# Kernel tuning notes

Measured on AMD Instinct MI355X. Metric: run time of the kernel, lower is better.

Reference implementation:

```python
import jax, jax.numpy as jnp
import numpy as np

EPS = 1e-8
XLAMBDA = 9.0  # hard-coded in i2t_scores call to Encoding_sim


def setup_inputs() -> dict:
    key = jax.random.key(0)
    ks = jax.random.split(key, 12)
    I, C, N, S, W, D = 48, 48, 1, 36, 32, 1024  # n_image, n_caption, views, regions, words, embed
    NB, HID, P, OUT, KK = 64, 256, 2, 1, 8      # num_block, hid_dim, Pieces, out_dim, n_kernels
    return {
        "images": jax.random.normal(ks[0], (I, N, S, D), jnp.float32),
        "captions": jax.random.normal(ks[1], (C, N, W, D), jnp.float32),
        "cap_lens": jax.random.randint(ks[2], (C,), 1, W + 1),
        "delt": jax.random.uniform(ks[3], (NB,), jnp.float32, 0.5, 1.0),
        "W1": jax.random.normal(ks[4], (NB, NB), jnp.float32) * 0.1,
        "b1": jnp.zeros((NB,), jnp.float32),
        "W2": jax.random.normal(ks[5], (NB, NB), jnp.float32) * 0.1,
        "b2": jnp.zeros((NB,), jnp.float32),
        "conv_W": jax.random.normal(ks[6], (KK, NB, NB), jnp.float32) * 0.1,
        "conv_b": jnp.zeros((NB,), jnp.float32),
        "Wm": jax.random.normal(ks[7], (NB, HID * P), jnp.float32) * 0.1,
        "bm": jnp.zeros((HID * P,), jnp.float32),
        "V": jax.random.normal(ks[8], (OUT, HID), jnp.float32) * 0.1,
        "g": jnp.ones((OUT,), jnp.float32),
        "bo": jnp.zeros((OUT,), jnp.float32),
    }


def _one_view(img, cap, delt, W1, b1, W2, b2, conv_W, conv_b, Wm, bm, V, g, bo):
    # img: (I, S, D) regions; cap: (C, W, D) words. All captions processed at full
    # length (the torch double loop over captions/views is fully vectorized).
    I, S, D = img.shape
    C = cap.shape[0]
    NB = delt.shape[0]
    db = D // NB
    # inter_relations with K=caption words, Q=image regions
    a = jax.nn.leaky_relu(jnp.einsum('cwd,isd->ciws', cap, img), 0.1)  # (C,I,W,S)
    a = a / (jnp.sqrt(jnp.sum(a * a, axis=-1, keepdims=True)) + EPS)   # l2norm over regions (dim=2)
    attn = jax.nn.softmax(XLAMBDA * jnp.swapaxes(a, -1, -2), axis=-1)  # (C,I,S,W) softmax over words
    # weighted caption context per region
    ctx = jnp.einsum('cisw,cwd->cisd', attn, cap)                      # (C,I,S,D)
    # blockwise cosine similarity vector, scaled by learned delt
    q = img.reshape(I, S, NB, db)[None]                                # (1,I,S,NB,db)
    cb = ctx.reshape(C, I, S, NB, db)
    w12 = jnp.sum(q * cb, axis=-1)
    nrm = jnp.linalg.norm(q, axis=-1) * jnp.linalg.norm(cb, axis=-1)
    sim = (w12 / jnp.maximum(nrm, EPS)) * delt                         # (C,I,S,NB)
    # WeightNetwork: learned region-region adjacency
    f1 = sim @ W1.T + b1
    f2 = sim @ W2.T + b2
    gw = jax.nn.softmax(jnp.einsum('cisn,citn->cist', f1, f2), axis=-1)  # (C,I,S,S)
    # VisualConvolution message passing: aggregate neighbors, mix with kernel bank
    msg = jnp.einsum('cist,citn->cisn', gw, sim)                       # (C,I,S,NB)
    conv = jnp.einsum('cisn,knm->cism', msg, conv_W) / conv_W.shape[0] + conv_b
    # MeanOut: linear to hid*Pieces, mean over pieces
    HID = V.shape[1]
    P = Wm.shape[1] // HID
    h = (conv @ Wm + bm).reshape(C, I, S, HID, P).mean(axis=-1)        # (C,I,S,HID)
    # weight-normalized output linear + tanh, then mean over regions
    Wn = g[:, None] * V / jnp.linalg.norm(V, axis=1, keepdims=True)
    y = jnp.tanh(h @ Wn.T + bo)                                        # (C,I,S,OUT)
    return jnp.mean(y.reshape(C, I, -1), axis=-1).T                    # (I,C)


def reference(images, captions, cap_lens, delt, W1, b1, W2, b2, conv_W, conv_b,
              Wm, bm, V, g, bo):
    # cap_lens: the ragged per-caption loop is uniformized to max length (see notes)
    f = lambda img, cap: _one_view(img, cap, delt, W1, b1, W2, b2, conv_W, conv_b,
                                   Wm, bm, V, g, bo)
    return jax.vmap(f, in_axes=(1, 1))(images, captions)  # (N, n_image, n_caption)
```

## Files before the change

### kernel.cpp

```cpp
#include <hip/hip_runtime.h>

#define EPSF 1e-8f

constexpr int NI = 48, NC = 48, S = 36, W = 32, D = 1024, NB = 64;
constexpr int CH = 64;
constexpr int NCH = D / CH;

typedef _Float16 half8 __attribute__((ext_vector_type(8)));
typedef _Float16 half4 __attribute__((ext_vector_type(4)));
typedef float f32x4 __attribute__((ext_vector_type(4)));

__device__ __forceinline__ f32x4 mfma16(half8 a, half8 b, f32x4 c) {
  return __builtin_amdgcn_mfma_f32_16x16x32_f16(a, b, c, 0, 0, 0);
}

constexpr size_t OFF_CAPTH = 17408;
constexpr size_t SZ_CAPT   = (size_t)48 * 32 * 1024 * 2;
constexpr size_t OFF_CAPTL = OFF_CAPTH + SZ_CAPT;
constexpr size_t OFF_L     = OFF_CAPTL + SZ_CAPT;
constexpr size_t SZ_L      = (size_t)1536 * 1728 * 4;
constexpr size_t OFF_DQ    = OFF_L + SZ_L;
constexpr size_t SZ_DQ     = (size_t)48 * 64 * 36 * 4;
constexpr size_t WS_NEED   = OFF_DQ + SZ_DQ;

__global__ __launch_bounds__(256) void prep_kernel(
    const float* __restrict__ W1, const float* __restrict__ b1,
    const float* __restrict__ W2,
    const float* __restrict__ convW, const float* __restrict__ convB,
    const float* __restrict__ Wm, const float* __restrict__ bm,
    const float* __restrict__ V, const float* __restrict__ g,
    const float* __restrict__ bo, float* __restrict__ ws) {
  __shared__ float sW1[64][68];
  __shared__ float sW2[64][68];
  __shared__ float wn[256];
  __shared__ float wv[64];
  __shared__ float vscale;
  const int t = threadIdx.x;
  for (int q = t; q < 2048; q += 256) {
    const int m = q >> 10, r = (q >> 4) & 63, c4 = (q & 15) * 4;
    const float* src = (m == 0 ? W1 : W2) + r * 64 + c4;
    float4 v = *reinterpret_cast<const float4*>(src);
    float* dst = (m == 0) ? &sW1[r][c4] : &sW2[r][c4];
    dst[0] = v.x; dst[1] = v.y; dst[2] = v.z; dst[3] = v.w;
  }
  if (t == 0) {
    float s = 0.f;
    for (int h = 0; h < 256; ++h) s += V[h] * V[h];
    vscale = g[0] / sqrtf(s);
  }
  __syncthreads();
  wn[t] = V[t] * vscale;
  __syncthreads();
  if (t < 64) {
    float acc = 0.f;
    for (int h = 0; h < 256; ++h)
      acc += 0.5f * (Wm[t * 512 + 2 * h] + Wm[t * 512 + 2 * h + 1]) * wn[h];
    wv[t] = acc;
  }
  __syncthreads();
  if (t < 64) {
    float acc = 0.f;
    for (int m = 0; m < 64; ++m) {
      float ce = 0.f;
      for (int k = 0; k < 8; ++k) ce += convW[k * 4096 + t * 64 + m];
      acc += 0.125f * ce * wv[m];
    }
    ws[t] = acc;
  }
  if (t == 0) {
    float bh = 0.f;
    for (int h = 0; h < 256; ++h) bh += 0.5f * (bm[2 * h] + bm[2 * h + 1]) * wn[h];
    float bc = 0.f;
    for (int m = 0; m < 64; ++m) bc += convB[m] * wv[m];
    ws[64] = bh + bc + bo[0];
  }
  if (t < 64) {
    float a = 0.f;
    for (int k = 0; k < 64; ++k) a += b1[k] * sW2[k][t];
    ws[66 + t] = a;
  }
  {
    const int i = t >> 2, j0 = (t & 3) * 16;
    float acc[16];
#pragma unroll
    for (int jj = 0; jj < 16; ++jj) acc[jj] = 0.f;
    for (int k = 0; k < 64; ++k) {
      const float w1v = sW1[k][i];
#pragma unroll
      for (int jj = 0; jj < 16; ++jj) acc[jj] += w1v * sW2[k][j0 + jj];
    }
    _Float16* wsM = reinterpret_cast<_Float16*>(ws + 132);
#pragma unroll
    for (int jj = 0; jj < 16; ++jj) {
      const float x = acc[jj];
      const _Float16 h = (_Float16)x;
      wsM[i * 64 + j0 + jj] = h;
      wsM[4096 + i * 64 + j0 + jj] = (_Float16)(x - (float)h);
    }
  }
}

__global__ __launch_bounds__(256) void setup_kernel(
    const float* __restrict__ captions, const float* __restrict__ images,
    const float* __restrict__ W1, const float* __restrict__ b1,
    const float* __restrict__ W2,
    const float* __restrict__ convW, const float* __restrict__ convB,
    const float* __restrict__ Wm, const float* __restrict__ bm,
    const float* __restrict__ V, const float* __restrict__ g,
    const float* __restrict__ bo,
    float* __restrict__ ws, _Float16* __restrict__ capTH,
    _Float16* __restrict__ capTL, float* __restrict__ dqT) {
  __shared__ union {
    struct { float sW1[64][68]; float sW2[64][68]; float wn[256]; float wv[64]; float vscale; } p;
    struct { _Float16 tH[64][40]; _Float16 tL[64][40]; } cc;
  } SM;
  const int t = threadIdx.x;
  const int bx = blockIdx.x;
  if (bx < 768) {
    const int c = bx >> 4, chn = bx & 15, d0 = chn * 64;
    for (int q = t; q < 512; q += 256) {
      const int w = q >> 4, c4 = (q & 15) * 4;
      const size_t gi = ((size_t)c * 32 + w) * 1024 + d0 + c4;
      float4 v = *reinterpret_cast<const float4*>(captions + gi);
      half4 hh, ll;
      hh[0] = (_Float16)v.x; ll[0] = (_Float16)(v.x - (float)hh[0]);
      hh[1] = (_Float16)v.y; ll[1] = (_Float16)(v.y - (float)hh[1]);
      hh[2] = (_Float16)v.z; ll[2] = (_Float16)(v.z - (float)hh[2]);
      hh[3] = (_Float16)v.w; ll[3] = (_Float16)(v.w - (float)hh[3]);
#pragma unroll
      for (int j = 0; j < 4; ++j) { SM.cc.tH[c4 + j][w] = hh[j]; SM.cc.tL[c4 + j][w] = ll[j]; }
    }
    __syncthreads();
    for (int q = t; q < 512; q += 256) {
      const int hl = q >> 8, dd = (q >> 2) & 63, w8 = (q & 3) * 8;
      half8 v = *reinterpret_cast<const half8*>(hl ? &SM.cc.tL[dd][w8] : &SM.cc.tH[dd][w8]);
      _Float16* dst = (hl ? capTL : capTH) + ((size_t)c * 1024 + d0 + dd) * 32 + w8;
      *reinterpret_cast<half8*>(dst) = v;
    }
  } else if (bx < 816) {
    const int i = bx - 768;
    for (int u = t; u < 2304; u += 256) {
      const int s = u >> 6, nb = u & 63;
      const float* p = images + ((size_t)i * 36 + s) * 1024 + nb * 16;
      float a = 0.f;
#pragma unroll
      for (int j = 0; j < 16; j += 4) {
        f32x4 v = *reinterpret_cast<const f32x4*>(p + j);
        a += v[0] * v[0] + v[1] * v[1] + v[2] * v[2] + v[3] * v[3];
      }
      dqT[((size_t)i * 64 + nb) * 36 + s] = a;
    }
  } else {
    for (int q = t; q < 2048; q += 256) {
      const int m = q >> 10, r = (q >> 4) & 63, c4 = (q & 15) * 4;
      const float* src = (m == 0 ? W1 : W2) + r * 64 + c4;
      float4 v = *reinterpret_cast<const float4*>(src);
      float* dst = (m == 0) ? &SM.p.sW1[r][c4] : &SM.p.sW2[r][c4];
      dst[0] = v.x; dst[1] = v.y; dst[2] = v.z; dst[3] = v.w;
    }
    if (t == 0) {
      float s = 0.f;
      for (int h = 0; h < 256; ++h) s += V[h] * V[h];
      SM.p.vscale = g[0] / sqrtf(s);
    }
    __syncthreads();
    SM.p.wn[t] = V[t] * SM.p.vscale;
    __syncthreads();
    if (t < 64) {
      float acc = 0.f;
      for (int h = 0; h < 256; ++h)
        acc += 0.5f * (Wm[t * 512 + 2 * h] + Wm[t * 512 + 2 * h + 1]) * SM.p.wn[h];
      SM.p.wv[t] = acc;
    }
    __syncthreads();
    if (t < 64) {
      float acc = 0.f;
      for (int m = 0; m < 64; ++m) {
        float ce = 0.f;
        for (int k = 0; k < 8; ++k) ce += convW[k * 4096 + t * 64 + m];
        acc += 0.125f * ce * SM.p.wv[m];
      }
      ws[t] = acc;
    }
    if (t == 0) {
      float bh = 0.f;
      for (int h = 0; h < 256; ++h) bh += 0.5f * (bm[2 * h] + bm[2 * h + 1]) * SM.p.wn[h];
      float bc = 0.f;
      for (int m = 0; m < 64; ++m) bc += convB[m] * SM.p.wv[m];
      ws[64] = bh + bc + bo[0];
    }
    if (t < 64) {
      float a = 0.f;
      for (int k = 0; k < 64; ++k) a += b1[k] * SM.p.sW2[k][t];
      ws[66 + t] = a;
    }
    {
      const int i = t >> 2, j0 = (t & 3) * 16;
      float acc[16];
#pragma unroll
      for (int jj = 0; jj < 16; ++jj) acc[jj] = 0.f;
      for (int k = 0; k < 64; ++k) {
        const float w1v = SM.p.sW1[k][i];
#pragma unroll
        for (int jj = 0; jj < 16; ++jj) acc[jj] += w1v * SM.p.sW2[k][j0 + jj];
      }
      _Float16* wsM = reinterpret_cast<_Float16*>(ws + 132);
#pragma unroll
      for (int jj = 0; jj < 16; ++jj) {
        const float x = acc[jj];
        const _Float16 h = (_Float16)x;
        wsM[i * 64 + j0 + jj] = h;
        wsM[4096 + i * 64 + j0 + jj] = (_Float16)(x - (float)h);
      }
    }
  }
}

__global__ __launch_bounds__(256, 3) void gemmL(
    const float* __restrict__ captions, const float* __restrict__ images,
    float* __restrict__ L) {
  __shared__ _Float16 sA[2][64][72];
  __shared__ _Float16 sB[2][96][72];
  const int t = threadIdx.x;
  const int lane = t & 63, wid = t >> 6;
  const int c = lane & 15, g = lane >> 4;
  const int bm = blockIdx.x / 18, bn = blockIdx.x % 18;
  const int m0 = bm * 64, n0 = bn * 96;
  const int wm = wid & 1, wn = wid >> 1;

  f32x4 acc[2][3] = {};
  f32x4 pfA[4], pfB[6];
  auto LD = [&](int ch) {
#pragma unroll
    for (int k = 0; k < 4; ++k) {
      const int u = t + k * 256;
      const int row = u >> 4, c4 = (u & 15) * 4;
      pfA[k] = *reinterpret_cast<const f32x4*>(captions + (size_t)(m0 + row) * 1024 + ch * 64 + c4);
    }
#pragma unroll
    for (int k = 0; k < 6; ++k) {
      const int u = t + k * 256;
      const int row = u >> 4, c4 = (u & 15) * 4;
      pfB[k] = *reinterpret_cast<const f32x4*>(images + (size_t)(n0 + row) * 1024 + ch * 64 + c4);
    }
  };
  auto ST = [&]() {
#pragma unroll
    for (int k = 0; k < 4; ++k) {
      const int u = t + k * 256;
      const int row = u >> 4, c4 = (u & 15) * 4;
      half4 hh, ll;
#pragma unroll
      for (int j = 0; j < 4; ++j) {
        const float x = pfA[k][j];
        hh[j] = (_Float16)x;
        ll[j] = (_Float16)(x - (float)hh[j]);
      }
      *reinterpret_cast<half4*>(&sA[0][row][c4]) = hh;
      *reinterpret_cast<half4*>(&sA[1][row][c4]) = ll;
    }
#pragma unroll
    for (int k = 0; k < 6; ++k) {
      const int u = t + k * 256;
      const int row = u >> 4, c4 = (u & 15) * 4;
      half4 hh, ll;
#pragma unroll
      for (int j = 0; j < 4; ++j) {
        const float x = pfB[k][j];
        hh[j] = (_Float16)x;
        ll[j] = (_Float16)(x - (float)hh[j]);
      }
      *reinterpret_cast<half4*>(&sB[0][row][c4]) = hh;
      *reinterpret_cast<half4*>(&sB[1][row][c4]) = ll;
    }
  };
  LD(0);
  for (int ch = 0; ch < NCH; ++ch) {
    __syncthreads();
    ST();
    if (ch < NCH - 1) LD(ch + 1);
    __syncthreads();
#pragma unroll
    for (int ks = 0; ks < 2; ++ks) {
      const int ko = ks * 32 + g * 8;
      half8 ah[2], al[2], bh[3], bl[3];
#pragma unroll
      for (int mt = 0; mt < 2; ++mt) {
        ah[mt] = *reinterpret_cast<const half8*>(&sA[0][wm * 32 + mt * 16 + c][ko]);
        al[mt] = *reinterpret_cast<const half8*>(&sA[1][wm * 32 + mt * 16 + c][ko]);
      }
#pragma unroll
      for (int nt = 0; nt < 3; ++nt) {
        bh[nt] = *reinterpret_cast<const half8*>(&sB[0][wn * 48 + nt * 16 + c][ko]);
        bl[nt] = *reinterpret_cast<const half8*>(&sB[1][wn * 48 + nt * 16 + c][ko]);
      }
#pragma unroll
      for (int mt = 0; mt < 2; ++mt)
#pragma unroll
        for (int nt = 0; nt < 3; ++nt) {
          acc[mt][nt] = mfma16(ah[mt], bh[nt], acc[mt][nt]);
          acc[mt][nt] = mfma16(ah[mt], bl[nt], acc[mt][nt]);
          acc[mt][nt] = mfma16(al[mt], bh[nt], acc[mt][nt]);
        }
    }
  }
#pragma unroll
  for (int mt = 0; mt < 2; ++mt)
#pragma unroll
    for (int nt = 0; nt < 3; ++nt)
#pragma unroll
      for (int r = 0; r < 4; ++r) {
        const int m = m0 + wm * 32 + mt * 16 + 4 * g + r;
        const int n = n0 + wn * 48 + nt * 16 + c;
        float x = acc[mt][nt][r];
        x = x > 0.f ? x : 0.1f * x;
        L[(size_t)m * 1728 + n] = x;
      }
}

__device__ __forceinline__ int swz(int row, int nbyte) {
  return row * 128 + (nbyte ^ ((row & 7) << 4));
}

__global__ __launch_bounds__(256, 5) void i2t_sim4(
    const float* __restrict__ images,
    const _Float16* __restrict__ capTH, const _Float16* __restrict__ capTL,
    const float* __restrict__ L, const float* __restrict__ dqT,
    const float* __restrict__ delt, const float* __restrict__ ws,
    float* __restrict__ out) {
  __shared__ union {
    float La[32][41];
    _Float16 yhl[2][2304];
  } UA;
  __shared__ union {
    _Float16 attn[2][36][40];
    float G[36][49];
  } UB;
  __shared__ _Float16 simS[2][2304];
  __shared__ float wrcp[32];
  __shared__ float sDelt[64], sCv[64], sU[64];
  __shared__ float sP[36], sScv[36], sRed[36];
  __shared__ float sBconst;

  const int t = threadIdx.x;
  const int lane = t & 63, wid = t >> 6;
  const int c = lane & 15, g = lane >> 4;
  const int bid = blockIdx.x;
  const int xcd = bid & 7, l = bid >> 3;
  const int ci = (xcd >> 1) * 12 + (l % 12);
  const int ii = (xcd & 1) * 24 + (l / 12);

  if (t < 64) { sDelt[t] = delt[t]; sCv[t] = ws[t]; sU[t] = ws[66 + t]; }
  if (t == 64) sBconst = ws[64];

#pragma unroll
  for (int k = 0; k < 2; ++k) {
    const int u = t + k * 256;
    if (u < 288) {
      const int w = u / 9, q4 = (u % 9) * 4;
      f32x4 x = *reinterpret_cast<const f32x4*>(
          L + (size_t)(ci * 32 + w) * 1728 + (size_t)ii * 36 + q4);
      *reinterpret_cast<f32x4*>(&UA.La[w][q4]) = x;
    }
  }
  __syncthreads();
  if (t < 32) {
    float s = 0.f;
    for (int ss = 0; ss < 36; ++ss) { const float v = UA.La[t][ss]; s += v * v; }
    wrcp[t] = 1.f / (sqrtf(s) + EPSF);
  }
  __syncthreads();
  if (t < 36) {
    float lw[32];
    float m = -1e30f;
#pragma unroll
    for (int w = 0; w < 32; ++w) {
      const float v = 9.f * UA.La[w][t] * wrcp[w];
      lw[w] = v;
      m = fmaxf(m, v);
    }
    float sum = 0.f;
#pragma unroll
    for (int w = 0; w < 32; ++w) { lw[w] = expf(lw[w] - m); sum += lw[w]; }
    const float r = 1.f / sum;
#pragma unroll
    for (int w = 0; w < 32; ++w) {
      const float a = lw[w] * r;
      const _Float16 h = (_Float16)a;
      UB.attn[0][t][w] = h;
      UB.attn[1][t][w] = (_Float16)(a - (float)h);
    }
  }
  __syncthreads();

  const size_t abase = ((size_t)ci * 1024 + wid * 16 + c) * 32 + g * 8;
  half8 pAh = *reinterpret_cast<const half8*>(capTH + abase);
  half8 pAl = *reinterpret_cast<const half8*>(capTL + abase);
  const float* pq[3];
  int scl[3];
  const float* pdqB = dqT + (size_t)ii * 64 * 36;
#pragma unroll
  for (int mt = 0; mt < 3; ++mt) {
    int s = mt * 16 + c; if (s > 35) s = 35;
    scl[mt] = s;
    pq[mt] = images + ((size_t)ii * 36 + s) * 1024 + wid * 16 + 4 * g;
  }
#pragma unroll 1
  for (int ch = 0; ch < 16; ++ch) {
    const half8 Ah = pAh, Al = pAl;
    if (ch < 15) {
      const size_t nx = abase + (size_t)(ch + 1) * 64 * 32;
      pAh = *reinterpret_cast<const half8*>(capTH + nx);
      pAl = *reinterpret_cast<const half8*>(capTL + nx);
    }
    const int nb = ch * 4 + wid;
    f32x4 qv[3];
    float dqv[3];
#pragma unroll
    for (int mt = 0; mt < 3; ++mt) {
      qv[mt] = *reinterpret_cast<const f32x4*>(pq[mt] + ch * 64);
      dqv[mt] = pdqB[(size_t)nb * 36 + scl[mt]];
    }
    float dts[3], dcs[3];
#pragma unroll
    for (int mt = 0; mt < 3; ++mt) {
      const half8 bh = *reinterpret_cast<const half8*>(&UB.attn[0][scl[mt]][g * 8]);
      const half8 bl = *reinterpret_cast<const half8*>(&UB.attn[1][scl[mt]][g * 8]);
      f32x4 a = {0.f, 0.f, 0.f, 0.f};
      a = mfma16(Ah, bh, a);
      a = mfma16(Ah, bl, a);
      a = mfma16(Al, bh, a);
      const f32x4 q = qv[mt];
      dts[mt] = a[0] * q[0] + a[1] * q[1] + a[2] * q[2] + a[3] * q[3];
      dcs[mt] = a[0] * a[0] + a[1] * a[1] + a[2] * a[2] + a[3] * a[3];
    }
#pragma unroll
    for (int mt = 0; mt < 3; ++mt) {
      float dt = dts[mt], dc = dcs[mt];
      dt += __shfl_xor(dt, 16); dc += __shfl_xor(dc, 16);
      dt += __shfl_xor(dt, 32); dc += __shfl_xor(dc, 32);
      const int s = mt * 16 + c;
      if (g == 0 && s < S) {
        const float r = __frsqrt_rn(fmaxf(dqv[mt] * dc, 1e-16f));
        const float sm = dt * r * sDelt[nb];
        const _Float16 h = (_Float16)sm;
        char* sb0 = (char*)&simS[0][0];
        char* sb1 = (char*)&simS[1][0];
        *reinterpret_cast<_Float16*>(sb0 + swz(s, nb * 2)) = h;
        *reinterpret_cast<_Float16*>(sb1 + swz(s, nb * 2)) = (_Float16)(sm - (float)h);
      }
    }
  }
  __syncthreads();

  const _Float16* wsM = reinterpret_cast<const _Float16*>(ws + 132);
  const char* sb0 = (const char*)&simS[0][0];
  const char* sb1 = (const char*)&simS[1][0];
  char* yb0 = (char*)&UA.yhl[0][0];
  char* yb1 = (char*)&UA.yhl[1][0];
  for (int tid = wid; tid < 12; tid += 4) {
    const int mt = tid >> 2, nt = tid & 3;
    f32x4 a = {0.f, 0.f, 0.f, 0.f};
#pragma unroll
    for (int ks = 0; ks < 2; ++ks) {
      const int ko = ks * 32 + g * 8;
      int ar = mt * 16 + c; if (ar > 35) ar = 35;
      half8 a_h = *reinterpret_cast<const half8*>(sb0 + swz(ar, ko * 2));
      half8 a_l = *reinterpret_cast<const half8*>(sb1 + swz(ar, ko * 2));
      half8 b_h = *reinterpret_cast<const half8*>(wsM + (nt * 16 + c) * 64 + ko);
      half8 b_l = *reinterpret_cast<const half8*>(wsM + 4096 + (nt * 16 + c) * 64 + ko);
      a = mfma16(a_h, b_h, a);
      a = mfma16(a_h, b_l, a);
      a = mfma16(a_l, b_h, a);
    }
#pragma unroll
    for (int r = 0; r < 4; ++r) {
      const int srow = mt * 16 + 4 * g + r;
      const int icol = nt * 16 + c;
      if (srow < S) {
        const float x = a[r];
        const _Float16 h = (_Float16)x;
        *reinterpret_cast<_Float16*>(yb0 + swz(srow, icol * 2)) = h;
        *reinterpret_cast<_Float16*>(yb1 + swz(srow, icol * 2)) = (_Float16)(x - (float)h);
      }
    }
  }
  if (t < 36) {
    float a = 0.f, b = 0.f;
#pragma unroll
    for (int k8 = 0; k8 < 8; ++k8) {
      half8 v0 = *reinterpret_cast<const half8*>(sb0 + swz(t, k8 * 16));
      half8 v1 = *reinterpret_cast<const half8*>(sb1 + swz(t, k8 * 16));
#pragma unroll
      for (int j = 0; j < 8; ++j) {
        const float sv = (float)v0[j] + (float)v1[j];
        a += sv * sU[k8 * 8 + j];
        b += sv * sCv[k8 * 8 + j];
      }
    }
    sP[t] = a;
    sScv[t] = b;
  }
  __syncthreads();
  for (int tid = wid; tid < 9; tid += 4) {
    const int mt = tid / 3, nt = tid % 3;
    f32x4 a = {0.f, 0.f, 0.f, 0.f};
#pragma unroll
    for (int ks = 0; ks < 2; ++ks) {
      const int ko = ks * 32 + g * 8;
      int ar = mt * 16 + c; if (ar > 35) ar = 35;
      int br = nt * 16 + c; if (br > 35) br = 35;
      half8 a_h = *reinterpret_cast<const half8*>(sb0 + swz(ar, ko * 2));
      half8 a_l = *reinterpret_cast<const half8*>(sb1 + swz(ar, ko * 2));
      half8 b_h = *reinterpret_cast<const half8*>((const char*)yb0 + swz(br, ko * 2));
      half8 b_l = *reinterpret_cast<const half8*>((const char*)yb1 + swz(br, ko * 2));
      a = mfma16(a_h, b_h, a);
      a = mfma16(a_h, b_l, a);
      a = mfma16(a_l, b_h, a);
    }
#pragma unroll
    for (int r = 0; r < 4; ++r) {
      const int srow = mt * 16 + 4 * g + r;
      const int tcol = nt * 16 + c;
      if (srow < S) UB.G[srow][tcol] = a[r];
    }
  }
  __syncthreads();
  if (t < 36) {
    float lg[36];
    float m = -1e30f;
#pragma unroll
    for (int t2 = 0; t2 < S; ++t2) {
      lg[t2] = UB.G[t][t2] + sP[t2];
      m = fmaxf(m, lg[t2]);
    }
    float se = 0.f, sv = 0.f;
#pragma unroll
    for (int t2 = 0; t2 < S; ++t2) {
      const float e = expf(lg[t2] - m);
      se += e; sv += e * sScv[t2];
    }
    sRed[t] = tanhf(sv / se + sBconst);
  }
  __syncthreads();
  if (t == 0) {
    float a = 0.f;
    for (int s = 0; s < S; ++s) a += sRed[s];
    out[(size_t)ii * NC + ci] = a * (1.f / 36.f);
  }
}

constexpr int ST1 = CH + 8;
constexpr int STT = 56;
constexpr int STI = 68;
constexpr int STC = 52;
constexpr int STH = 72;
constexpr int STA = 40;

__global__ __launch_bounds__(256, 2) void i2t_fb(
    const float* __restrict__ images, const float* __restrict__ captions,
    const float* __restrict__ delt, const float* __restrict__ ws,
    float* __restrict__ out) {
  __shared__ union {
    struct { _Float16 cap[2][32][ST1]; _Float16 img[2][48][ST1]; } s1;
    float lpart[4][32][36];
    struct { _Float16 capT[2][64][STT]; float img32[36][STI]; } s2;
    _Float16 M[2][64][STH];
    float G[36][52];
  } rA;
  __shared__ union {
    float La[32][37];
    float ctxT[64][STC];
    _Float16 yhl[2][48][STH];
  } rB;
  __shared__ _Float16 attn_hl[2][48][STA];
  __shared__ _Float16 sim_hl[2][48][STH];
  __shared__ float wrcp[32];
  __shared__ float sDelt[64], sCv[64], sU[64];
  __shared__ float sP[36], sScv[36], sRed[36];
  __shared__ float sBconst;

  const int t = threadIdx.x;
  const int lane = t & 63, wid = t >> 6;
  const int mrow = lane & 15, grp = lane >> 4;
  const int bid = blockIdx.x;
  const int xcd = bid & 7, l = bid >> 3;
  const int ci = (xcd >> 1) * 12 + (l % 12);
  const int ii = (xcd & 1) * 24 + (l / 12);
  const float* cap = captions + ci * (W * D);
  const float* img = images + ii * (S * D);
  const f32x4 zero4 = {0.f, 0.f, 0.f, 0.f};

  if (t < 64) { sDelt[t] = delt[t]; sCv[t] = ws[t]; sU[t] = ws[66 + t]; }
  if (t == 64) sBconst = ws[64];

  f32x4 acc1[2][3];
#pragma unroll
  for (int mt = 0; mt < 2; ++mt)
#pragma unroll
    for (int nt = 0; nt < 3; ++nt) acc1[mt][nt] = zero4;

  for (int ch = 0; ch < NCH; ++ch) {
    const int d0 = ch * CH;
    __syncthreads();
    for (int q = t; q < 1088; q += 256) {
      const int row = q >> 4, c4 = (q & 15) * 4;
      const float* src = (row < 32) ? (cap + row * D + d0 + c4)
                                    : (img + (row - 32) * D + d0 + c4);
      float4 v = *reinterpret_cast<const float4*>(src);
      half4 hh, ll;
      hh[0] = (_Float16)v.x; ll[0] = (_Float16)(v.x - (float)hh[0]);
      hh[1] = (_Float16)v.y; ll[1] = (_Float16)(v.y - (float)hh[1]);
      hh[2] = (_Float16)v.z; ll[2] = (_Float16)(v.z - (float)hh[2]);
      hh[3] = (_Float16)v.w; ll[3] = (_Float16)(v.w - (float)hh[3]);
      _Float16* dh = (row < 32) ? &rA.s1.cap[0][row][c4] : &rA.s1.img[0][row - 32][c4];
      _Float16* dl = (row < 32) ? &rA.s1.cap[1][row][c4] : &rA.s1.img[1][row - 32][c4];
      *reinterpret_cast<half4*>(dh) = hh;
      *reinterpret_cast<half4*>(dl) = ll;
    }
    __syncthreads();
    if ((ch & 3) == wid) {
#pragma unroll
      for (int ks = 0; ks < 2; ++ks) {
        const int ko = ks * 32 + grp * 8;
        half8 ah[2], al[2], bh[3], bl[3];
#pragma unroll
        for (int mt = 0; mt < 2; ++mt) {
          ah[mt] = *reinterpret_cast<const half8*>(&rA.s1.cap[0][mt * 16 + mrow][ko]);
          al[mt] = *reinterpret_cast<const half8*>(&rA.s1.cap[1][mt * 16 + mrow][ko]);
        }
#pragma unroll
        for (int nt = 0; nt < 3; ++nt) {
          bh[nt] = *reinterpret_cast<const half8*>(&rA.s1.img[0][nt * 16 + mrow][ko]);
          bl[nt] = *reinterpret_cast<const half8*>(&rA.s1.img[1][nt * 16 + mrow][ko]);
        }
#pragma unroll
        for (int mt = 0; mt < 2; ++mt)
#pragma unroll
          for (int nt = 0; nt < 3; ++nt) {
            acc1[mt][nt] = mfma16(ah[mt], bh[nt], acc1[mt][nt]);
            acc1[mt][nt] = mfma16(ah[mt], bl[nt], acc1[mt][nt]);
            acc1[mt][nt] = mfma16(al[mt], bh[nt], acc1[mt][nt]);
          }
      }
    }
  }
  __syncthreads();
#pragma unroll
  for (int mt = 0; mt < 2; ++mt)
#pragma unroll
    for (int nt = 0; nt < 3; ++nt)
#pragma unroll
      for (int r = 0; r < 4; ++r) {
        const int w = mt * 16 + grp * 4 + r;
        const int s = nt * 16 + mrow;
        if (s < S) rA.lpart[wid][w][s] = acc1[mt][nt][r];
      }
  __syncthreads();
  {
    const float* lp = &rA.lpart[0][0][0];
    for (int e = t; e < W * S; e += 256) {
      float x = lp[e] + lp[e + 1152] + lp[e + 2304] + lp[e + 3456];
      x = x > 0.f ? x : 0.1f * x;
      rB.La[e / S][e % S] = x;
    }
  }
  __syncthreads();
  if (t < W) {
    float sum = 0.f;
    for (int s = 0; s < S; ++s) { float v = rB.La[t][s]; sum += v * v; }
    wrcp[t] = 1.f / (sqrtf(sum) + EPSF);
  }
  __syncthreads();
  if (t < S) {
    float lw[32];
    float m = -1e30f;
#pragma unroll
    for (int w = 0; w < 32; ++w) {
      float v = 9.f * rB.La[w][t] * wrcp[w];
      lw[w] = v;
      m = fmaxf(m, v);
    }
    float sum = 0.f;
#pragma unroll
    for (int w = 0; w < 32; ++w) { lw[w] = expf(lw[w] - m); sum += lw[w]; }
    const float r = 1.f / sum;
#pragma unroll
    for (int w = 0; w < 32; ++w) {
      float a = lw[w] * r;
      _Float16 h = (_Float16)a;
      attn_hl[0][t][w] = h;
      attn_hl[1][t][w] = (_Float16)(a - (float)h);
    }
  }
  __syncthreads();

  half8 a2h[3], a2l[3];
#pragma unroll
  for (int mt = 0; mt < 3; ++mt) {
    a2h[mt] = *reinterpret_cast<const half8*>(&attn_hl[0][mt * 16 + mrow][grp * 8]);
    a2l[mt] = *reinterpret_cast<const half8*>(&attn_hl[1][mt * 16 + mrow][grp * 8]);
  }
  for (int ch = 0; ch < NCH; ++ch) {
    const int d0 = ch * CH;
    __syncthreads();
    {
      const int dl = t & 63, wb = (t >> 6) * 8;
      half8 hh, ll;
#pragma unroll
      for (int k = 0; k < 8; ++k) {
        float x = cap[(wb + k) * D + d0 + dl];
        hh[k] = (_Float16)x;
        ll[k] = (_Float16)(x - (float)hh[k]);
      }
      *reinterpret_cast<half8*>(&rA.s2.capT[0][dl][wb]) = hh;
      *reinterpret_cast<half8*>(&rA.s2.capT[1][dl][wb]) = ll;
    }
    for (int q = t; q < 576; q += 256) {
      const int sr = q >> 4, c4 = (q & 15) * 4;
      float4 v = *reinterpret_cast<const float4*>(img + sr * D + d0 + c4);
      *reinterpret_cast<float4*>(&rA.s2.img32[sr][c4]) = v;
    }
    __syncthreads();
    {
      const int dloc = wid * 16 + mrow;
      half8 b_h = *reinterpret_cast<const half8*>(&rA.s2.capT[0][dloc][grp * 8]);
      half8 b_l = *reinterpret_cast<const half8*>(&rA.s2.capT[1][dloc][grp * 8]);
#pragma unroll
      for (int mt = 0; mt < 3; ++mt) {
        f32x4 acc = zero4;
        acc = mfma16(a2h[mt], b_h, acc);
        acc = mfma16(a2h[mt], b_l, acc);
        acc = mfma16(a2l[mt], b_h, acc);
        const int s0 = mt * 16 + grp * 4;
        if (s0 < S) *reinterpret_cast<f32x4*>(&rB.ctxT[dloc][s0]) = acc;
      }
    }
    __syncthreads();
    if (t < 144) {
      const int s = t % 36, nbl = t / 36;
      const int n = ch * 4 + nbl;
      float dt = 0.f, dc = 0.f, dq = 0.f;
#pragma unroll
      for (int j4 = 0; j4 < 4; ++j4) {
        f32x4 qv = *reinterpret_cast<const f32x4*>(&rA.s2.img32[s][nbl * 16 + j4 * 4]);
#pragma unroll
        for (int jj = 0; jj < 4; ++jj) {
          float cx = rB.ctxT[nbl * 16 + j4 * 4 + jj][s];
          float q = qv[jj];
          dt += q * cx; dc += cx * cx; dq += q * q;
        }
      }
      float sim = dt / fmaxf(sqrtf(dq) * sqrtf(dc), EPSF) * sDelt[n];
      _Float16 h = (_Float16)sim;
      sim_hl[0][s][n] = h;
      sim_hl[1][s][n] = (_Float16)(sim - (float)h);
    }
  }
  __syncthreads();

  for (int q = t; q < 1024; q += 256) {
    const int hl = q >> 9, row = (q >> 3) & 63, c8 = (q & 7) * 8;
    const _Float16* wsM = reinterpret_cast<const _Float16*>(ws + 132);
    *reinterpret_cast<half8*>(&rA.M[hl][row][c8]) =
        *reinterpret_cast<const half8*>(wsM + hl * 4096 + row * 64 + c8);
  }
  __syncthreads();
  for (int tid = wid; tid < 12; tid += 4) {
    const int mt = tid >> 2, nt = tid & 3;
    f32x4 acc = zero4;
#pragma unroll
    for (int ks = 0; ks < 2; ++ks) {
      const int ko = ks * 32 + grp * 8;
      half8 a_h = *reinterpret_cast<const half8*>(&sim_hl[0][mt * 16 + mrow][ko]);
      half8 a_l = *reinterpret_cast<const half8*>(&sim_hl[1][mt * 16 + mrow][ko]);
      half8 b_h = *reinterpret_cast<const half8*>(&rA.M[0][nt * 16 + mrow][ko]);
      half8 b_l = *reinterpret_cast<const half8*>(&rA.M[1][nt * 16 + mrow][ko]);
      acc = mfma16(a_h, b_h, acc);
      acc = mfma16(a_h, b_l, acc);
      acc = mfma16(a_l, b_h, acc);
    }
#pragma unroll
    for (int r = 0; r < 4; ++r) {
      const int srow = mt * 16 + grp * 4 + r;
      const int icol = nt * 16 + mrow;
      float x = acc[r];
      _Float16 h = (_Float16)x;
      rB.yhl[0][srow][icol] = h;
      rB.yhl[1][srow][icol] = (_Float16)(x - (float)h);
    }
  }
  __syncthreads();
  for (int tid = wid; tid < 9; tid += 4) {
    const int mt = tid / 3, nt = tid % 3;
    f32x4 acc = zero4;
#pragma unroll
    for (int ks = 0; ks < 2; ++ks) {
      const int ko = ks * 32 + grp * 8;
      half8 a_h = *reinterpret_cast<const half8*>(&sim_hl[0][mt * 16 + mrow][ko]);
      half8 a_l = *reinterpret_cast<const half8*>(&sim_hl[1][mt * 16 + mrow][ko]);
      half8 b_h = *reinterpret_cast<const half8*>(&rB.yhl[0][nt * 16 + mrow][ko]);
      half8 b_l = *reinterpret_cast<const half8*>(&rB.yhl[1][nt * 16 + mrow][ko]);
      acc = mfma16(a_h, b_h, acc);
      acc = mfma16(a_h, b_l, acc);
      acc = mfma16(a_l, b_h, acc);
    }
#pragma unroll
    for (int r = 0; r < 4; ++r) {
      const int srow = mt * 16 + grp * 4 + r;
      const int tcol = nt * 16 + mrow;
      if (srow < S) rA.G[srow][tcol] = acc[r];
    }
  }
  __syncthreads();
  if (t < S) {
    float a = 0.f;
#pragma unroll
    for (int n = 0; n < 64; ++n)
      a += ((float)sim_hl[0][t][n] + (float)sim_hl[1][t][n]) * sU[n];
    sP[t] = a;
  } else if (t >= 64 && t < 64 + S) {
    const int r = t - 64;
    float a = 0.f;
#pragma unroll
    for (int n = 0; n < 64; ++n)
      a += ((float)sim_hl[0][r][n] + (float)sim_hl[1][r][n]) * sCv[n];
    sScv[r] = a;
  }
  __syncthreads();
  if (t < S) {
    float lg[36];
    float m = -1e30f;
#pragma unroll
    for (int t2 = 0; t2 < S; ++t2) {
      lg[t2] = rA.G[t][t2] + sP[t2];
      m = fmaxf(m, lg[t2]);
    }
    float se = 0.f, sv = 0.f;
#pragma unroll
    for (int t2 = 0; t2 < S; ++t2) {
      float e = expf(lg[t2] - m);
      se += e; sv += e * sScv[t2];
    }
    sRed[t] = tanhf(sv / se + sBconst);
  }
  __syncthreads();
  if (t == 0) {
    float a = 0.f;
    for (int s = 0; s < S; ++s) a += sRed[s];
    out[ii * NC + ci] = a * (1.f / 36.f);
  }
}

extern "C" void kernel_launch(void* const* d_in, const int* in_sizes, int n_in,
                              void* d_out, int out_size, void* d_ws, size_t ws_size,
                              hipStream_t stream) {
  const float* images   = (const float*)d_in[0];
  const float* captions = (const float*)d_in[1];
  const float* delt  = (const float*)d_in[3];
  const float* W1    = (const float*)d_in[4];
  const float* b1    = (const float*)d_in[5];
  const float* W2    = (const float*)d_in[6];
  const float* convW = (const float*)d_in[8];
  const float* convB = (const float*)d_in[9];
  const float* Wm    = (const float*)d_in[10];
  const float* bm    = (const float*)d_in[11];
  const float* V     = (const float*)d_in[12];
  const float* g     = (const float*)d_in[13];
  const float* bo    = (const float*)d_in[14];
  float* ws  = (float*)d_ws;
  float* out = (float*)d_out;

  if (ws_size >= WS_NEED) {
    char* base = (char*)d_ws;
    _Float16* capTH = (_Float16*)(base + OFF_CAPTH);
    _Float16* capTL = (_Float16*)(base + OFF_CAPTL);
    float*    Lbuf  = (float*)(base + OFF_L);
    float*    dqT   = (float*)(base + OFF_DQ);
    setup_kernel<<<dim3(817), 256, 0, stream>>>(captions, images, W1, b1, W2,
                                                convW, convB, Wm, bm, V, g, bo,
                                                ws, capTH, capTL, dqT);
    gemmL<<<dim3(432), 256, 0, stream>>>(captions, images, Lbuf);
    i2t_sim4<<<dim3(2304), 256, 0, stream>>>(images, capTH, capTL, Lbuf, dqT,
                                             delt, ws, out);
  } else {
    prep_kernel<<<1, 256, 0, stream>>>(W1, b1, W2, convW, convB, Wm, bm, V, g, bo, ws);
    i2t_fb<<<dim3(NI * NC), 256, 0, stream>>>(images, captions, delt, ws, out);
  }
}
```

Before: 160.9 us.

## Fuse setup and L-GEMM kernels; accumulate block sims via LDS atomics

```diff
diff --git a/kernel.cpp b/kernel.cpp
--- a/kernel.cpp
+++ b/kernel.cpp
@@ -20,7 +20,7 @@
 constexpr size_t OFF_L     = OFF_CAPTL + SZ_CAPT;
 constexpr size_t SZ_L      = (size_t)1536 * 1728 * 4;
 constexpr size_t OFF_DQ    = OFF_L + SZ_L;
-constexpr size_t SZ_DQ     = (size_t)48 * 64 * 36 * 4;
+constexpr size_t SZ_DQ     = (size_t)48 * 36 * 64 * 4;
 constexpr size_t WS_NEED   = OFF_DQ + SZ_DQ;
 
 __global__ __launch_bounds__(256) void prep_kernel(
@@ -100,7 +100,7 @@
   }
 }
 
-__global__ __launch_bounds__(256) void setup_kernel(
+__global__ __launch_bounds__(256, 3) void fused_pre(
     const float* __restrict__ captions, const float* __restrict__ images,
     const float* __restrict__ W1, const float* __restrict__ b1,
     const float* __restrict__ W2,
@@ -109,15 +109,114 @@
     const float* __restrict__ V, const float* __restrict__ g,
     const float* __restrict__ bo,
     float* __restrict__ ws, _Float16* __restrict__ capTH,
-    _Float16* __restrict__ capTL, float* __restrict__ dqT) {
+    _Float16* __restrict__ capTL, float* __restrict__ dqT,
+    float* __restrict__ L) {
   __shared__ union {
+    struct { _Float16 sA[2][64][72]; _Float16 sB[2][96][72]; } gm;
     struct { float sW1[64][68]; float sW2[64][68]; float wn[256]; float wv[64]; float vscale; } p;
     struct { _Float16 tH[64][40]; _Float16 tL[64][40]; } cc;
-  } SM;
+  } U;
   const int t = threadIdx.x;
   const int bx = blockIdx.x;
-  if (bx < 768) {
-    const int c = bx >> 4, chn = bx & 15, d0 = chn * 64;
+
+  if (bx < 432) {
+    const int lane = t & 63, wid = t >> 6;
+    const int c = lane & 15, g2 = lane >> 4;
+    const int bm = bx / 18, bn = bx % 18;
+    const int m0 = bm * 64, n0 = bn * 96;
+    const int wm = wid & 1, wn = wid >> 1;
+
+    f32x4 acc[2][3] = {};
+    f32x4 pfA[4], pfB[6];
+    auto LD = [&](int ch) {
+#pragma unroll
+      for (int k = 0; k < 4; ++k) {
+        const int u = t + k * 256;
+        const int row = u >> 4, c4 = (u & 15) * 4;
+        pfA[k] = *reinterpret_cast<const f32x4*>(captions + (size_t)(m0 + row) * 1024 + ch * 64 + c4);
+      }
+#pragma unroll
+      for (int k = 0; k < 6; ++k) {
+        const int u = t + k * 256;
+        const int row = u >> 4, c4 = (u & 15) * 4;
+        pfB[k] = *reinterpret_cast<const f32x4*>(images + (size_t)(n0 + row) * 1024 + ch * 64 + c4);
+      }
+    };
+    auto ST = [&]() {
+#pragma unroll
+      for (int k = 0; k < 4; ++k) {
+        const int u = t + k * 256;
+        const int row = u >> 4, c4 = (u & 15) * 4;
+        half4 hh, ll;
+#pragma unroll
+        for (int j = 0; j < 4; ++j) {
+          const float x = pfA[k][j];
+          hh[j] = (_Float16)x;
+          ll[j] = (_Float16)(x - (float)hh[j]);
+        }
+        *reinterpret_cast<half4*>(&U.gm.sA[0][row][c4]) = hh;
+        *reinterpret_cast<half4*>(&U.gm.sA[1][row][c4]) = ll;
+      }
+#pragma unroll
+      for (int k = 0; k < 6; ++k) {
+        const int u = t + k * 256;
+        const int row = u >> 4, c4 = (u & 15) * 4;
+        half4 hh, ll;
+#pragma unroll
+        for (int j = 0; j < 4; ++j) {
+          const float x = pfB[k][j];
+          hh[j] = (_Float16)x;
+          ll[j] = (_Float16)(x - (float)hh[j]);
+        }
+        *reinterpret_cast<half4*>(&U.gm.sB[0][row][c4]) = hh;
+        *reinterpret_cast<half4*>(&U.gm.sB[1][row][c4]) = ll;
+      }
+    };
+    LD(0);
+    for (int ch = 0; ch < NCH; ++ch) {
+      __syncthreads();
+      ST();
+      if (ch < NCH - 1) LD(ch + 1);
+      __syncthreads();
+#pragma unroll
+      for (int ks = 0; ks < 2; ++ks) {
+        const int ko = ks * 32 + g2 * 8;
+        half8 ah[2], al[2], bh[3], bl[3];
+#pragma unroll
+        for (int mt = 0; mt < 2; ++mt) {
+          ah[mt] = *reinterpret_cast<const half8*>(&U.gm.sA[0][wm * 32 + mt * 16 + c][ko]);
+          al[mt] = *reinterpret_cast<const half8*>(&U.gm.sA[1][wm * 32 + mt * 16 + c][ko]);
+        }
+#pragma unroll
+        for (int nt = 0; nt < 3; ++nt) {
+          bh[nt] = *reinterpret_cast<const half8*>(&U.gm.sB[0][wn * 48 + nt * 16 + c][ko]);
+          bl[nt] = *reinterpret_cast<const half8*>(&U.gm.sB[1][wn * 48 + nt * 16 + c][ko]);
+        }
+#pragma unroll
+        for (int mt = 0; mt < 2; ++mt)
+#pragma unroll
+          for (int nt = 0; nt < 3; ++nt) {
+            acc[mt][nt] = mfma16(ah[mt], bh[nt], acc[mt][nt]);
+            acc[mt][nt] = mfma16(ah[mt], bl[nt], acc[mt][nt]);
+            acc[mt][nt] = mfma16(al[mt], bh[nt], acc[mt][nt]);
+          }
+      }
+    }
+#pragma unroll
+    for (int mt = 0; mt < 2; ++mt)
+#pragma unroll
+      for (int nt = 0; nt < 3; ++nt)
+#pragma unroll
+        for (int r = 0; r < 4; ++r) {
+          const int m = m0 + wm * 32 + mt * 16 + 4 * g2 + r;
+          const int n = n0 + wn * 48 + nt * 16 + c;
+          float x = acc[mt][nt][r];
+          x = x > 0.f ? x : 0.1f * x;
+          L[(size_t)m * 1728 + n] = x;
+        }
+  } else if (bx < 1200) {
+    const int b2 = bx - 432;
+    const int c = b2 >> 4, chn = b2 & 15, d0 = chn * 64;
     for (int q = t; q < 512; q += 256) {
       const int w = q >> 4, c4 = (q & 15) * 4;
       const size_t gi = ((size_t)c * 32 + w) * 1024 + d0 + c4;
@@ -128,17 +227,17 @@
       hh[2] = (_Float16)v.z; ll[2] = (_Float16)(v.z - (float)hh[2]);
       hh[3] = (_Float16)v.w; ll[3] = (_Float16)(v.w - (float)hh[3]);
 #pragma unroll
-      for (int j = 0; j < 4; ++j) { SM.cc.tH[c4 + j][w] = hh[j]; SM.cc.tL[c4 + j][w] = ll[j]; }
+      for (int j = 0; j < 4; ++j) { U.cc.tH[c4 + j][w] = hh[j]; U.cc.tL[c4 + j][w] = ll[j]; }
     }
     __syncthreads();
     for (int q = t; q < 512; q += 256) {
       const int hl = q >> 8, dd = (q >> 2) & 63, w8 = (q & 3) * 8;
-      half8 v = *reinterpret_cast<const half8*>(hl ? &SM.cc.tL[dd][w8] : &SM.cc.tH[dd][w8]);
+      half8 v = *reinterpret_cast<const half8*>(hl ? &U.cc.tL[dd][w8] : &U.cc.tH[dd][w8]);
       _Float16* dst = (hl ? capTL : capTH) + ((size_t)c * 1024 + d0 + dd) * 32 + w8;
       *reinterpret_cast<half8*>(dst) = v;
     }
-  } else if (bx < 816) {
-    const int i = bx - 768;
+  } else if (bx < 1248) {
+    const int i = bx - 1200;
     for (int u = t; u < 2304; u += 256) {
       const int s = u >> 6, nb = u & 63;
       const float* p = images + ((size_t)i * 36 + s) * 1024 + nb * 16;
@@ -148,29 +247,29 @@
         f32x4 v = *reinterpret_cast<const f32x4*>(p + j);
         a += v[0] * v[0] + v[1] * v[1] + v[2] * v[2] + v[3] * v[3];
       }
-      dqT[((size_t)i * 64 + nb) * 36 + s] = a;
+      dqT[((size_t)i * 36 + s) * 64 + nb] = a;
     }
   } else {
     for (int q = t; q < 2048; q += 256) {
       const int m = q >> 10, r = (q >> 4) & 63, c4 = (q & 15) * 4;
       const float* src = (m == 0 ? W1 : W2) + r * 64 + c4;
       float4 v = *reinterpret_cast<const float4*>(src);
-      float* dst = (m == 0) ? &SM.p.sW1[r][c4] : &SM.p.sW2[r][c4];
+      float* dst = (m == 0) ? &U.p.sW1[r][c4] : &U.p.sW2[r][c4];
       dst[0] = v.x; dst[1] = v.y; dst[2] = v.z; dst[3] = v.w;
     }
     if (t == 0) {
       float s = 0.f;
       for (int h = 0; h < 256; ++h) s += V[h] * V[h];
-      SM.p.vscale = g[0] / sqrtf(s);
+      U.p.vscale = g[0] / sqrtf(s);
     }
     __syncthreads();
-    SM.p.wn[t] = V[t] * SM.p.vscale;
+    U.p.wn[t] = V[t] * U.p.vscale;
     __syncthreads();
     if (t < 64) {
       float acc = 0.f;
       for (int h = 0; h < 256; ++h)
-        acc += 0.5f * (Wm[t * 512 + 2 * h] + Wm[t * 512 + 2 * h + 1]) * SM.p.wn[h];
-      SM.p.wv[t] = acc;
+        acc += 0.5f * (Wm[t * 512 + 2 * h] + Wm[t * 512 + 2 * h + 1]) * U.p.wn[h];
+      U.p.wv[t] = acc;
     }
     __syncthreads();
     if (t < 64) {
@@ -178,20 +277,20 @@
       for (int m = 0; m < 64; ++m) {
         float ce = 0.f;
         for (int k = 0; k < 8; ++k) ce += convW[k * 4096 + t * 64 + m];
-        acc += 0.125f * ce * SM.p.wv[m];
+        acc += 0.125f * ce * U.p.wv[m];
       }
       ws[t] = acc;
     }
     if (t == 0) {
       float bh = 0.f;
-      for (int h = 0; h < 256; ++h) bh += 0.5f * (bm[2 * h] + bm[2 * h + 1]) * SM.p.wn[h];
+      for (int h = 0; h < 256; ++h) bh += 0.5f * (bm[2 * h] + bm[2 * h + 1]) * U.p.wn[h];
       float bc = 0.f;
-      for (int m = 0; m < 64; ++m) bc += convB[m] * SM.p.wv[m];
+      for (int m = 0; m < 64; ++m) bc += convB[m] * U.p.wv[m];
       ws[64] = bh + bc + bo[0];
     }
     if (t < 64) {
       float a = 0.f;
-      for (int k = 0; k < 64; ++k) a += b1[k] * SM.p.sW2[k][t];
+      for (int k = 0; k < 64; ++k) a += b1[k] * U.p.sW2[k][t];
       ws[66 + t] = a;
     }
     {
@@ -200,9 +299,9 @@
 #pragma unroll
       for (int jj = 0; jj < 16; ++jj) acc[jj] = 0.f;
       for (int k = 0; k < 64; ++k) {
-        const float w1v = SM.p.sW1[k][i];
-#pragma unroll
-        for (int jj = 0; jj < 16; ++jj) acc[jj] += w1v * SM.p.sW2[k][j0 + jj];
+        const float w1v = U.p.sW1[k][i];
+#pragma unroll
+        for (int jj = 0; jj < 16; ++jj) acc[jj] += w1v * U.p.sW2[k][j0 + jj];
       }
       _Float16* wsM = reinterpret_cast<_Float16*>(ws + 132);
 #pragma unroll
@@ -216,113 +315,11 @@
   }
 }
 
-__global__ __launch_bounds__(256, 3) void gemmL(
-    const float* __restrict__ captions, const float* __restrict__ images,
-    float* __restrict__ L) {
-  __shared__ _Float16 sA[2][64][72];
-  __shared__ _Float16 sB[2][96][72];
-  const int t = threadIdx.x;
-  const int lane = t & 63, wid = t >> 6;
-  const int c = lane & 15, g = lane >> 4;
-  const int bm = blockIdx.x / 18, bn = blockIdx.x % 18;
-  const int m0 = bm * 64, n0 = bn * 96;
-  const int wm = wid & 1, wn = wid >> 1;
-
-  f32x4 acc[2][3] = {};
-  f32x4 pfA[4], pfB[6];
-  auto LD = [&](int ch) {
-#pragma unroll
-    for (int k = 0; k < 4; ++k) {
-      const int u = t + k * 256;
-      const int row = u >> 4, c4 = (u & 15) * 4;
-      pfA[k] = *reinterpret_cast<const f32x4*>(captions + (size_t)(m0 + row) * 1024 + ch * 64 + c4);
-    }
-#pragma unroll
-    for (int k = 0; k < 6; ++k) {
-      const int u = t + k * 256;
-      const int row = u >> 4, c4 = (u & 15) * 4;
-      pfB[k] = *reinterpret_cast<const f32x4*>(images + (size_t)(n0 + row) * 1024 + ch * 64 + c4);
-    }
-  };
-  auto ST = [&]() {
-#pragma unroll
-    for (int k = 0; k < 4; ++k) {
-      const int u = t + k * 256;
-      const int row = u >> 4, c4 = (u & 15) * 4;
-      half4 hh, ll;
-#pragma unroll
-      for (int j = 0; j < 4; ++j) {
-        const float x = pfA[k][j];
-        hh[j] = (_Float16)x;
-        ll[j] = (_Float16)(x - (float)hh[j]);
-      }
-      *reinterpret_cast<half4*>(&sA[0][row][c4]) = hh;
-      *reinterpret_cast<half4*>(&sA[1][row][c4]) = ll;
-    }
-#pragma unroll
-    for (int k = 0; k < 6; ++k) {
-      const int u = t + k * 256;
-      const int row = u >> 4, c4 = (u & 15) * 4;
-      half4 hh, ll;
-#pragma unroll
-      for (int j = 0; j < 4; ++j) {
-        const float x = pfB[k][j];
-        hh[j] = (_Float16)x;
-        ll[j] = (_Float16)(x - (float)hh[j]);
-      }
-      *reinterpret_cast<half4*>(&sB[0][row][c4]) = hh;
-      *reinterpret_cast<half4*>(&sB[1][row][c4]) = ll;
-    }
-  };
-  LD(0);
-  for (int ch = 0; ch < NCH; ++ch) {
-    __syncthreads();
-    ST();
-    if (ch < NCH - 1) LD(ch + 1);
-    __syncthreads();
-#pragma unroll
-    for (int ks = 0; ks < 2; ++ks) {
-      const int ko = ks * 32 + g * 8;
-      half8 ah[2], al[2], bh[3], bl[3];
-#pragma unroll
-      for (int mt = 0; mt < 2; ++mt) {
-        ah[mt] = *reinterpret_cast<const half8*>(&sA[0][wm * 32 + mt * 16 + c][ko]);
-        al[mt] = *reinterpret_cast<const half8*>(&sA[1][wm * 32 + mt * 16 + c][ko]);
-      }
-#pragma unroll
-      for (int nt = 0; nt < 3; ++nt) {
-        bh[nt] = *reinterpret_cast<const half8*>(&sB[0][wn * 48 + nt * 16 + c][ko]);
-        bl[nt] = *reinterpret_cast<const half8*>(&sB[1][wn * 48 + nt * 16 + c][ko]);
-      }
-#pragma unroll
-      for (int mt = 0; mt < 2; ++mt)
-#pragma unroll
-        for (int nt = 0; nt < 3; ++nt) {
-          acc[mt][nt] = mfma16(ah[mt], bh[nt], acc[mt][nt]);
-          acc[mt][nt] = mfma16(ah[mt], bl[nt], acc[mt][nt]);
-          acc[mt][nt] = mfma16(al[mt], bh[nt], acc[mt][nt]);
-        }
-    }
-  }
-#pragma unroll
-  for (int mt = 0; mt < 2; ++mt)
-#pragma unroll
-    for (int nt = 0; nt < 3; ++nt)
-#pragma unroll
-      for (int r = 0; r < 4; ++r) {
-        const int m = m0 + wm * 32 + mt * 16 + 4 * g + r;
-        const int n = n0 + wn * 48 + nt * 16 + c;
-        float x = acc[mt][nt][r];
-        x = x > 0.f ? x : 0.1f * x;
-        L[(size_t)m * 1728 + n] = x;
-      }
-}
-
 __device__ __forceinline__ int swz(int row, int nbyte) {
   return row * 128 + (nbyte ^ ((row & 7) << 4));
 }
 
-__global__ __launch_bounds__(256, 5) void i2t_sim4(
+__global__ __launch_bounds__(256, 4) void i2t_sim5(
     const float* __restrict__ images,
     const _Float16* __restrict__ capTH, const _Float16* __restrict__ capTL,
     const float* __restrict__ L, const float* __restrict__ dqT,
@@ -330,6 +327,7 @@
     float* __restrict__ out) {
   __shared__ union {
     float La[32][41];
+    float dtdc[36][64][2];
     _Float16 yhl[2][2304];
   } UA;
   __shared__ union {
@@ -393,12 +391,16 @@
   }
   __syncthreads();
 
+  for (int k = lane; k < 36 * 16 * 2; k += 64) {
+    const int x = k & 1, nbk = (k >> 1) & 15, s = k >> 5;
+    UA.dtdc[s][nbk * 4 + wid][x] = 0.f;
+  }
+
   const size_t abase = ((size_t)ci * 1024 + wid * 16 + c) * 32 + g * 8;
   half8 pAh = *reinterpret_cast<const half8*>(capTH + abase);
   half8 pAl = *reinterpret_cast<const half8*>(capTL + abase);
   const float* pq[3];
   int scl[3];
-  const float* pdqB = dqT + (size_t)ii * 64 * 36;
 #pragma unroll
   for (int mt = 0; mt < 3; ++mt) {
     int s = mt * 16 + c; if (s > 35) s = 35;
@@ -414,41 +416,40 @@
       pAl = *reinterpret_cast<const half8*>(capTL + nx);
     }
     const int nb = ch * 4 + wid;
-    f32x4 qv[3];
-    float dqv[3];
 #pragma unroll
     for (int mt = 0; mt < 3; ++mt) {
-      qv[mt] = *reinterpret_cast<const f32x4*>(pq[mt] + ch * 64);
-      dqv[mt] = pdqB[(size_t)nb * 36 + scl[mt]];
-    }
-    float dts[3], dcs[3];
-#pragma unroll
-    for (int mt = 0; mt < 3; ++mt) {
+      const f32x4 q = *reinterpret_cast<const f32x4*>(pq[mt] + ch * 64);
       const half8 bh = *reinterpret_cast<const half8*>(&UB.attn[0][scl[mt]][g * 8]);
       const half8 bl = *reinterpret_cast<const half8*>(&UB.attn[1][scl[mt]][g * 8]);
       f32x4 a = {0.f, 0.f, 0.f, 0.f};
       a = mfma16(Ah, bh, a);
       a = mfma16(Ah, bl, a);
       a = mfma16(Al, bh, a);
-      const f32x4 q = qv[mt];
-      dts[mt] = a[0] * q[0] + a[1] * q[1] + a[2] * q[2] + a[3] * q[3];
-      dcs[mt] = a[0] * a[0] + a[1] * a[1] + a[2] * a[2] + a[3] * a[3];
-    }
-#pragma unroll
-    for (int mt = 0; mt < 3; ++mt) {
-      float dt = dts[mt], dc = dcs[mt];
-      dt += __shfl_xor(dt, 16); dc += __shfl_xor(dc, 16);
-      dt += __shfl_xor(dt, 32); dc += __shfl_xor(dc, 32);
+      const float dt = a[0] * q[0] + a[1] * q[1] + a[2] * q[2] + a[3] * q[3];
+      const float dc = a[0] * a[0] + a[1] * a[1] + a[2] * a[2] + a[3] * a[3];
       const int s = mt * 16 + c;
-      if (g == 0 && s < S) {
-        const float r = __frsqrt_rn(fmaxf(dqv[mt] * dc, 1e-16f));
-        const float sm = dt * r * sDelt[nb];
-        const _Float16 h = (_Float16)sm;
-        char* sb0 = (char*)&simS[0][0];
-        char* sb1 = (char*)&simS[1][0];
-        *reinterpret_cast<_Float16*>(sb0 + swz(s, nb * 2)) = h;
-        *reinterpret_cast<_Float16*>(sb1 + swz(s, nb * 2)) = (_Float16)(sm - (float)h);
-      }
+      if (s < S) {
+        atomicAdd(&UA.dtdc[s][nb][0], dt);
+        atomicAdd(&UA.dtdc[s][nb][1], dc);
+      }
+    }
+  }
+  __syncthreads();
+
+  {
+    char* sb0 = (char*)&simS[0][0];
+    char* sb1 = (char*)&simS[1][0];
+    const float* pdq = dqT + (size_t)ii * 2304;
+    for (int u = t; u < 36 * 64; u += 256) {
+      const int s = u >> 6, nb = u & 63;
+      const float dt = UA.dtdc[s][nb][0];
+      const float dc = UA.dtdc[s][nb][1];
+      const float dq = pdq[u];
+      const float r = __frsqrt_rn(fmaxf(dq * dc, 1e-16f));
+      const float sm = dt * r * sDelt[nb];
+      const _Float16 h = (_Float16)sm;
+      *reinterpret_cast<_Float16*>(sb0 + swz(s, nb * 2)) = h;
+      *reinterpret_cast<_Float16*>(sb1 + swz(s, nb * 2)) = (_Float16)(sm - (float)h);
     }
   }
   __syncthreads();
@@ -877,11 +878,10 @@
     _Float16* capTL = (_Float16*)(base + OFF_CAPTL);
     float*    Lbuf  = (float*)(base + OFF_L);
     float*    dqT   = (float*)(base + OFF_DQ);
-    setup_kernel<<<dim3(817), 256, 0, stream>>>(captions, images, W1, b1, W2,
-                                                convW, convB, Wm, bm, V, g, bo,
-                                                ws, capTH, capTL, dqT);
-    gemmL<<<dim3(432), 256, 0, stream>>>(captions, images, Lbuf);
-    i2t_sim4<<<dim3(2304), 256, 0, stream>>>(images, capTH, capTL, Lbuf, dqT,
+    fused_pre<<<dim3(1249), 256, 0, stream>>>(captions, images, W1, b1, W2,
+                                              convW, convB, Wm, bm, V, g, bo,
+                                              ws, capTH, capTL, dqT, Lbuf);
+    i2t_sim5<<<dim3(2304), 256, 0, stream>>>(images, capTH, capTL, Lbuf, dqT,
                                              delt, ws, out);
   } else {
     prep_kernel<<<1, 256, 0, stream>>>(W1, b1, W2, convW, convB, Wm, bm, V, g, bo, ws);
```

New measurement: 299.2 us. 1.86x slower.
